# Optimization experiments

Measured on AMD Instinct MI355X. Metric: run time of the kernel, lower is better.

## Reference

```python
import jax, jax.numpy as jnp
import numpy as np

NUM_USERS = 100000
NUM_ITEMS = 50000
N_NODES = NUM_USERS + NUM_ITEMS
EMBED_DIM = 64
NUM_LAYERS = 3
N_EDGES = 1000000


def setup_inputs() -> dict:
    key = jax.random.key(0)
    k1, k2 = jax.random.split(key)
    edge_index = jax.random.randint(k1, (2, N_EDGES), 0, N_NODES, dtype=jnp.int64)
    # xavier_uniform for Embedding weight [N, d]
    limit = float(np.sqrt(6.0 / (N_NODES + EMBED_DIM)))
    emb_weight = jax.random.uniform(k2, (N_NODES, EMBED_DIM), dtype=jnp.float32,
                                    minval=-limit, maxval=limit)
    return {"edge_index": edge_index, "emb_weight": emb_weight}


def _lgconv(x, src, dst, norm):
    # out[dst] += norm * x[src]  (degree-normalized scatter-add)
    msgs = x[src] * norm[:, None]              # [E, d]
    return jax.ops.segment_sum(msgs, dst, num_segments=N_NODES)


def reference(edge_index, emb_weight):
    src, dst = edge_index[0], edge_index[1]
    # gcn_norm with add_self_loops=False: deg over target (col) index
    deg = jax.ops.segment_sum(jnp.ones((N_EDGES,), emb_weight.dtype), dst,
                              num_segments=N_NODES)
    dinv = jnp.where(deg > 0, jax.lax.rsqrt(jnp.maximum(deg, 1.0)), 0.0)
    norm = dinv[src] * dinv[dst]               # [E]

    emb = emb_weight
    acc = emb                                   # running sum over layer outputs
    for _ in range(NUM_LAYERS):
        emb = _lgconv(emb, src, dst, norm)
        acc = acc + emb
    out = acc / (NUM_LAYERS + 1)                # mean over stacked layer embeddings
    user_emb = out[:NUM_USERS]
    item_emb = out[NUM_USERS:]
    return (user_emb, item_emb)
```

## Files before the change

kernel.cpp:

```cpp
#include <hip/hip_runtime.h>
#include <hip/hip_fp16.h>


constexpr int kNodes     = 150000;
constexpr int kDim       = 64;
constexpr int kEdges     = 1000000;
constexpr int kEmbFloats = kNodes * kDim;
constexpr int kBkt       = (kNodes + 255) / 256;
constexpr int kBktCap    = 2048;
constexpr int kChunk     = 4096;

typedef float  floatx4 __attribute__((ext_vector_type(4)));

__device__ __forceinline__ int wave_incl_scan(int v, int lane) {
    #pragma unroll
    for (int s = 1; s < 64; s <<= 1) {
        int u = __shfl_up(v, s);
        if (lane >= s) v += u;
    }
    return v;
}

#define ACC_LO(s, r) asm("v_fma_mix_f32 %0, %1, 1.0, %0 op_sel:[0,0,0] op_sel_hi:[1,0,0]" : "+v"(s) : "v"(r))
#define ACC_HI(s, r) asm("v_fma_mix_f32 %0, %1, 1.0, %0 op_sel:[1,0,0] op_sel_hi:[1,0,0]" : "+v"(s) : "v"(r))

#define ACC_ROW(rr) do { \
    ACC_LO(s0, rr.x); ACC_HI(s1, rr.x); \
    ACC_LO(s2, rr.y); ACC_HI(s3, rr.y); \
    ACC_LO(s4, rr.z); ACC_HI(s5, rr.z); \
    ACC_LO(s6, rr.w); ACC_HI(s7, rr.w); } while (0)


__global__ __launch_bounds__(1024) void binA_kernel(const int* __restrict__ src,
                                                    const int* __restrict__ dst,
                                                    int* __restrict__ cur,
                                                    unsigned* __restrict__ bin) {
    __shared__ int hist[1024];
    __shared__ int cursor[1024];
    __shared__ int sexcl[1024];
    __shared__ int gstart[1024];
    __shared__ int wsum[16];
    __shared__ unsigned staged[kChunk];
    __shared__ unsigned short sbkt[kChunk];

    int t      = threadIdx.x;
    int lane   = t & 63;
    int w      = t >> 6;
    int chunk0 = blockIdx.x * kChunk;
    int n      = min(kChunk, kEdges - chunk0);

    hist[t] = 0;
    __syncthreads();

    int myb[4], myd[4];
    #pragma unroll
    for (int j = 0; j < 4; ++j) {
        int i = j * 1024 + t;
        if (i < n) {
            int d = dst[chunk0 + i];
            myb[j] = d >> 8;
            myd[j] = d & 255;
            atomicAdd(&hist[myb[j]], 1);
        } else myb[j] = -1;
    }
    __syncthreads();

    int c   = hist[t];
    int inc = wave_incl_scan(c, lane);
    if (lane == 63) wsum[w] = inc;
    __syncthreads();
    if (w == 0) {
        int v  = (lane < 16) ? wsum[lane] : 0;
        int sc = wave_incl_scan(v, lane);
        if (lane < 16) wsum[lane] = sc - v;
    }
    __syncthreads();
    int excl = wsum[w] + inc - c;
    sexcl[t]  = excl;
    cursor[t] = excl;
    if (t < kBkt) gstart[t] = atomicAdd(&cur[t], c);
    __syncthreads();

    #pragma unroll
    for (int j = 0; j < 4; ++j) {
        int i = j * 1024 + t;
        if (i < n) {
            int s = src[chunk0 + i];
            unsigned pk = ((unsigned)myd[j] << 24) | (unsigned)s;
            int p = atomicAdd(&cursor[myb[j]], 1);
            staged[p] = pk;
            sbkt[p]   = (unsigned short)myb[j];
        }
    }
    __syncthreads();

    #pragma unroll
    for (int j = 0; j < 4; ++j) {
        int i = j * 1024 + t;
        if (i < n) {
            int bu = sbkt[i];
            int gp = gstart[bu] + (i - sexcl[bu]);
            if (gp < kBktCap) bin[(size_t)bu * kBktCap + gp] = staged[i];
        }
    }
}


__global__ __launch_bounds__(256) void binB_kernel(const int* __restrict__ cur,
                                                   const unsigned* __restrict__ bin,
                                                   int* __restrict__ pairs,
                                                   int2* __restrict__ offcnt,
                                                   int* __restrict__ order,
                                                   const float4* __restrict__ emb4,
                                                   int4* __restrict__ y4) {
    __shared__ int lcnt[256];
    __shared__ int cursor[256];
    __shared__ int wsum[4];
    __shared__ int wred[4];
    __shared__ int chist[64];
    __shared__ int stage[kBktCap];
    __shared__ float sdinv[256];

    int b = blockIdx.x;
    int t = threadIdx.x;
    int lane = t & 63, w = t >> 6;
    int cnt = min(cur[b], kBktCap);
    const unsigned* mybin = bin + (size_t)b * kBktCap;

    {
        int acc = 0;
        for (int j = t; j < b; j += 256) acc += min(cur[j], kBktCap);
        #pragma unroll
        for (int s = 32; s; s >>= 1) acc += __shfl_down(acc, s);
        if (lane == 0) wred[w] = acc;
    }

    lcnt[t] = 0;
    if (t < 64) chist[t] = 0;
    __syncthreads();
    int bs = wred[0] + wred[1] + wred[2] + wred[3];

    for (int i = t; i < cnt; i += 256) atomicAdd(&lcnt[mybin[i] >> 24], 1);
    __syncthreads();

    int c   = lcnt[t];
    int inc = wave_incl_scan(c, lane);
    if (lane == 63) wsum[w] = inc;
    int cv = min(c, 63);
    atomicAdd(&chist[cv], 1);
    __syncthreads();

    if (t < 64) {
        int v  = chist[t];
        int sc = wave_incl_scan(v, lane);
        chist[t] = sc - v;
    }
    if (t == 0) {
        int a = 0;
        #pragma unroll
        for (int k = 0; k < 4; ++k) { int v = wsum[k]; wsum[k] = a; a += v; }
    }
    __syncthreads();
    int excl = wsum[w] + inc - c;

    int node = (b << 8) + t;
    float dv = (c > 0) ? rsqrtf((float)c) : 0.0f;
    sdinv[t] = dv;
    if (node < kNodes) offcnt[node] = make_int2(bs + excl, c);
    cursor[t] = excl;

    {
        int slot = atomicAdd(&chist[cv], 1);
        order[(b << 8) + slot] = (node < kNodes) ? node : kNodes;
    }
    __syncthreads();

    for (int i = t; i < cnt; i += 256) {
        unsigned v = mybin[i];
        int p = atomicAdd(&cursor[v >> 24], 1);
        stage[p] = (int)(v & 0x00FFFFFFu);
    }
    __syncthreads();
    for (int i = t; i < cnt; i += 256) pairs[bs + i] = stage[i];

    #pragma unroll
    for (int k = 0; k < 8; ++k) {
        int idx   = (k << 8) + t;
        int nl    = idx >> 3;
        int node2 = (b << 8) + nl;
        int qq    = idx & 7;
        if (node2 < kNodes) {
            float d = sdinv[nl];
            size_t e = (size_t)node2 * 16 + (size_t)qq * 2;
            float4 v0 = emb4[e];
            float4 v1 = emb4[e + 1];
            __half2 p0 = __floats2half2_rn(v0.x * d, v0.y * d);
            __half2 p1 = __floats2half2_rn(v0.z * d, v0.w * d);
            __half2 p2 = __floats2half2_rn(v1.x * d, v1.y * d);
            __half2 p3 = __floats2half2_rn(v1.z * d, v1.w * d);
            int4 wv;
            wv.x = *reinterpret_cast<int*>(&p0); wv.y = *reinterpret_cast<int*>(&p1);
            wv.z = *reinterpret_cast<int*>(&p2); wv.w = *reinterpret_cast<int*>(&p3);
            y4[(size_t)node2 * 8 + qq] = wv;
        } else if (node2 == kNodes) {
            int4 z; z.x = 0; z.y = 0; z.z = 0; z.w = 0;
            y4[(size_t)node2 * 8 + qq] = z;
        }
    }
}


__global__ __launch_bounds__(256) void gather_kernel(const int2* __restrict__ offcnt,
                                                     const int* __restrict__ order,
                                                     const int* __restrict__ pairs,
                                                     const __half* __restrict__ x16,
                                                     __half* __restrict__ yOut,
                                                     const float4* __restrict__ emb4,
                                                     const __half* __restrict__ y1,
                                                     const __half* __restrict__ y2,
                                                     float* __restrict__ outf,
                                                     int mode) {
    int t    = blockIdx.x * 256 + threadIdx.x;
    int slot = t >> 3;
    int q    = t & 7;
    int node = order[slot];
    if (node == kNodes) {
        if (mode == 0) {
            int4 z; z.x = 0; z.y = 0; z.z = 0; z.w = 0;
            ((int4*)(yOut + ((size_t)kNodes << 6)))[q] = z;
        }
        return;
    }
    int lane = threadIdx.x & 63;
    int gb   = lane & 56;

    int2 oc = offcnt[node];
    int b = oc.x, cnt = oc.y;

    float s0 = 0.f, s1 = 0.f, s2 = 0.f, s3 = 0.f,
          s4 = 0.f, s5 = 0.f, s6 = 0.f, s7 = 0.f;

    int mysrc = (q < cnt) ? pairs[b + q] : kNodes;
    for (int base2 = 0; base2 < cnt; base2 += 8) {
        int np  = base2 + 8 + q;
        int nxt = (np < cnt) ? pairs[b + np] : kNodes;

        int si0 = __shfl(mysrc, gb + 0);
        int si1 = __shfl(mysrc, gb + 1);
        int si2 = __shfl(mysrc, gb + 2);
        int si3 = __shfl(mysrc, gb + 3);
        int si4 = __shfl(mysrc, gb + 4);
        int si5 = __shfl(mysrc, gb + 5);
        int si6 = __shfl(mysrc, gb + 6);
        int si7 = __shfl(mysrc, gb + 7);
        int4 r0 = *(const int4*)(x16 + ((size_t)si0 << 6) + (q << 3));
        int4 r1 = *(const int4*)(x16 + ((size_t)si1 << 6) + (q << 3));
        int4 r2 = *(const int4*)(x16 + ((size_t)si2 << 6) + (q << 3));
        int4 r3 = *(const int4*)(x16 + ((size_t)si3 << 6) + (q << 3));
        int4 r4 = *(const int4*)(x16 + ((size_t)si4 << 6) + (q << 3));
        int4 r5 = *(const int4*)(x16 + ((size_t)si5 << 6) + (q << 3));
        int4 r6 = *(const int4*)(x16 + ((size_t)si6 << 6) + (q << 3));
        int4 r7 = *(const int4*)(x16 + ((size_t)si7 << 6) + (q << 3));
        ACC_ROW(r0); ACC_ROW(r1); ACC_ROW(r2); ACC_ROW(r3);
        ACC_ROW(r4); ACC_ROW(r5); ACC_ROW(r6); ACC_ROW(r7);
        mysrc = nxt;
    }

    float dv = (cnt > 0) ? rsqrtf((float)cnt) : 0.0f;
    if (mode == 0) {
        float dv2 = dv * dv;
        __half2 p0 = __floats2half2_rn(s0 * dv2, s1 * dv2);
        __half2 p1 = __floats2half2_rn(s2 * dv2, s3 * dv2);
        __half2 p2 = __floats2half2_rn(s4 * dv2, s5 * dv2);
        __half2 p3 = __floats2half2_rn(s6 * dv2, s7 * dv2);
        int4 wv;
        wv.x = *reinterpret_cast<int*>(&p0); wv.y = *reinterpret_cast<int*>(&p1);
        wv.z = *reinterpret_cast<int*>(&p2); wv.w = *reinterpret_cast<int*>(&p3);
        ((int4*)(yOut + ((size_t)node << 6)))[q] = wv;
    } else {
        float sq = sqrtf((float)cnt);
        size_t i4 = (size_t)node * 16 + (size_t)q * 2;
        int4 r1 = ((const int4*)(y1 + ((size_t)node << 6)))[q];
        int4 r2 = ((const int4*)(y2 + ((size_t)node << 6)))[q];
        float4 e0 = emb4[i4];
        float4 e1 = emb4[i4 + 1];
        float2 a0 = __half22float2(*reinterpret_cast<__half2*>(&r1.x));
        float2 a1 = __half22float2(*reinterpret_cast<__half2*>(&r1.y));
        float2 a2 = __half22float2(*reinterpret_cast<__half2*>(&r1.z));
        float2 a3 = __half22float2(*reinterpret_cast<__half2*>(&r1.w));
        float2 c0 = __half22float2(*reinterpret_cast<__half2*>(&r2.x));
        float2 c1 = __half22float2(*reinterpret_cast<__half2*>(&r2.y));
        float2 c2 = __half22float2(*reinterpret_cast<__half2*>(&r2.z));
        float2 c3 = __half22float2(*reinterpret_cast<__half2*>(&r2.w));
        floatx4 o0, o1;
        o0.x = (e0.x + (a0.x + c0.x) * sq + s0 * dv) * 0.25f;
        o0.y = (e0.y + (a0.y + c0.y) * sq + s1 * dv) * 0.25f;
        o0.z = (e0.z + (a1.x + c1.x) * sq + s2 * dv) * 0.25f;
        o0.w = (e0.w + (a1.y + c1.y) * sq + s3 * dv) * 0.25f;
        o1.x = (e1.x + (a2.x + c2.x) * sq + s4 * dv) * 0.25f;
        o1.y = (e1.y + (a2.y + c2.y) * sq + s5 * dv) * 0.25f;
        o1.z = (e1.z + (a3.x + c3.x) * sq + s6 * dv) * 0.25f;
        o1.w = (e1.w + (a3.y + c3.y) * sq + s7 * dv) * 0.25f;
        floatx4* op = (floatx4*)(outf + i4 * 4);
        __builtin_nontemporal_store(o0, op);
        __builtin_nontemporal_store(o1, op + 1);
    }
}


extern "C" void kernel_launch(void* const* d_in, const int* in_sizes, int n_in,
                              void* d_out, int out_size, void* d_ws, size_t ws_size,
                              hipStream_t stream) {
    const int*   edge  = (const int*)d_in[0];
    const int*   src   = edge;
    const int*   dst   = edge + kEdges;
    const float* emb_w = (const float*)d_in[1];
    float*       out   = (float*)d_out;

    char*     ws      = (char*)d_ws;
    int*      cur     = (int*)(ws);
    int*      order   = (int*)(ws + 4096);
    int2*     offcnt  = (int2*)(ws + 604160);
    int*      pairs   = (int*)(ws + 1804160);
    unsigned* bin     = (unsigned*)(ws + 5804160);
    __half*   y0      = (__half*)(ws + 10604672);
    __half*   yA      = (__half*)(ws + 29804800);
    __half*   yB      = (__half*)(ws + 49004928);

    const int binABlocks   = (kEdges + kChunk - 1) / kChunk;
    const int gatherBlocks = (kBkt * 256 * 8) / 256;

    (void)hipMemsetAsync(cur, 0, (size_t)kBkt * 4, stream);
    binA_kernel<<<binABlocks, 1024, 0, stream>>>(src, dst, cur, bin);
    binB_kernel<<<kBkt, 256, 0, stream>>>(cur, bin, pairs, offcnt, order,
                                          (const float4*)emb_w, (int4*)y0);

    gather_kernel<<<gatherBlocks, 256, 0, stream>>>(offcnt, order, pairs, y0,
                                                    yA, nullptr, nullptr, nullptr,
                                                    nullptr, 0);
    gather_kernel<<<gatherBlocks, 256, 0, stream>>>(offcnt, order, pairs, yA,
                                                    yB, nullptr, nullptr, nullptr,
                                                    nullptr, 0);
    gather_kernel<<<gatherBlocks, 256, 0, stream>>>(offcnt, order, pairs, yB,
                                                    nullptr, (const float4*)emb_w,
                                                    yA, yB, out, 1);
}
```

Measured before the change: 218.4 us.

## Fuse binB and gather layers into cooperative kernel with slot-ordered embeddings

Merges the bin-finalize pass and the three gather layers into one cooperative persistent kernel separated by grid-wide syncs, removing four launches. Embeddings are now stored in degree-sorted slot order and the edge source indices are remapped to slots, so gather reads and writes run sequentially per slot instead of indirecting through node ids. The cost is an extra remap pass over the edges, grid-sync overhead, and a persistent grid limited by occupancy. The workspace is also reshuffled so the bin buffer aliases yA.

Measured after the change: 714.6 us. 227% more time.

```diff
diff --git a/kernel.cpp b/kernel.cpp
--- a/kernel.cpp
+++ b/kernel.cpp
@@ -1,12 +1,15 @@
 #include <hip/hip_runtime.h>
 #include <hip/hip_fp16.h>
+#include <hip/hip_cooperative_groups.h>
+
+namespace cg = cooperative_groups;
 
 
 constexpr int kNodes     = 150000;
 constexpr int kDim       = 64;
 constexpr int kEdges     = 1000000;
-constexpr int kEmbFloats = kNodes * kDim;
 constexpr int kBkt       = (kNodes + 255) / 256;
+constexpr int kSlots     = kBkt * 256;
 constexpr int kBktCap    = 2048;
 constexpr int kChunk     = 4096;
 
@@ -106,13 +109,16 @@
 }
 
 
-__global__ __launch_bounds__(256) void binB_kernel(const int* __restrict__ cur,
-                                                   const unsigned* __restrict__ bin,
-                                                   int* __restrict__ pairs,
-                                                   int2* __restrict__ offcnt,
-                                                   int* __restrict__ order,
-                                                   const float4* __restrict__ emb4,
-                                                   int4* __restrict__ y4) {
+__device__ __forceinline__ void phaseB(int b,
+                                       const int* __restrict__ cur,
+                                       const unsigned* __restrict__ bin,
+                                       int* __restrict__ pairs,
+                                       int2* __restrict__ offcnt,
+                                       int* __restrict__ order,
+                                       int* __restrict__ islot,
+                                       int* __restrict__ totalE,
+                                       const float4* __restrict__ emb4,
+                                       int4* __restrict__ y4) {
     __shared__ int lcnt[256];
     __shared__ int cursor[256];
     __shared__ int wsum[4];
@@ -120,8 +126,8 @@
     __shared__ int chist[64];
     __shared__ int stage[kBktCap];
     __shared__ float sdinv[256];
-
-    int b = blockIdx.x;
+    __shared__ int sslot[256];
+
     int t = threadIdx.x;
     int lane = t & 63, w = t >> 6;
     int cnt = min(cur[b], kBktCap);
@@ -166,13 +172,15 @@
     int node = (b << 8) + t;
     float dv = (c > 0) ? rsqrtf((float)c) : 0.0f;
     sdinv[t] = dv;
-    if (node < kNodes) offcnt[node] = make_int2(bs + excl, c);
     cursor[t] = excl;
 
-    {
-        int slot = atomicAdd(&chist[cv], 1);
-        order[(b << 8) + slot] = (node < kNodes) ? node : kNodes;
-    }
+    int myslot = atomicAdd(&chist[cv], 1);
+    sslot[t] = myslot;
+    int gslot = (b << 8) + myslot;
+    order[gslot]  = (node < kNodes) ? node : kNodes;
+    offcnt[gslot] = make_int2(bs + excl, c);
+    if (node <= kNodes) islot[node] = gslot;
+    if (b == kBkt - 1 && t == 0) *totalE = bs + cnt;
     __syncthreads();
 
     for (int i = t; i < cnt; i += 256) {
@@ -187,8 +195,9 @@
     for (int k = 0; k < 8; ++k) {
         int idx   = (k << 8) + t;
         int nl    = idx >> 3;
+        int qq    = idx & 7;
         int node2 = (b << 8) + nl;
-        int qq    = idx & 7;
+        size_t gs = (size_t)((b << 8) + sslot[nl]);
         if (node2 < kNodes) {
             float d = sdinv[nl];
             size_t e = (size_t)node2 * 16 + (size_t)qq * 2;
@@ -201,110 +210,144 @@
             int4 wv;
             wv.x = *reinterpret_cast<int*>(&p0); wv.y = *reinterpret_cast<int*>(&p1);
             wv.z = *reinterpret_cast<int*>(&p2); wv.w = *reinterpret_cast<int*>(&p3);
-            y4[(size_t)node2 * 8 + qq] = wv;
-        } else if (node2 == kNodes) {
+            y4[gs * 8 + qq] = wv;
+        } else {
             int4 z; z.x = 0; z.y = 0; z.z = 0; z.w = 0;
-            y4[(size_t)node2 * 8 + qq] = z;
-        }
-    }
-}
-
-
-__global__ __launch_bounds__(256) void gather_kernel(const int2* __restrict__ offcnt,
-                                                     const int* __restrict__ order,
-                                                     const int* __restrict__ pairs,
-                                                     const __half* __restrict__ x16,
-                                                     __half* __restrict__ yOut,
-                                                     const float4* __restrict__ emb4,
-                                                     const __half* __restrict__ y1,
-                                                     const __half* __restrict__ y2,
-                                                     float* __restrict__ outf,
-                                                     int mode) {
-    int t    = blockIdx.x * 256 + threadIdx.x;
-    int slot = t >> 3;
-    int q    = t & 7;
-    int node = order[slot];
-    if (node == kNodes) {
-        if (mode == 0) {
-            int4 z; z.x = 0; z.y = 0; z.z = 0; z.w = 0;
-            ((int4*)(yOut + ((size_t)kNodes << 6)))[q] = z;
-        }
-        return;
-    }
+            y4[gs * 8 + qq] = z;
+        }
+    }
+}
+
+
+__device__ __forceinline__ void gather_layer(const int2* __restrict__ offcnt,
+                                             const int* __restrict__ order,
+                                             const int* __restrict__ pairs,
+                                             const __half* __restrict__ x16,
+                                             __half* __restrict__ yOut,
+                                             const float4* __restrict__ emb4,
+                                             const __half* __restrict__ y1,
+                                             const __half* __restrict__ y2,
+                                             float* __restrict__ outf,
+                                             int padslot, int mode) {
+    int q    = threadIdx.x & 7;
     int lane = threadIdx.x & 63;
     int gb   = lane & 56;
 
-    int2 oc = offcnt[node];
-    int b = oc.x, cnt = oc.y;
-
-    float s0 = 0.f, s1 = 0.f, s2 = 0.f, s3 = 0.f,
-          s4 = 0.f, s5 = 0.f, s6 = 0.f, s7 = 0.f;
-
-    int mysrc = (q < cnt) ? pairs[b + q] : kNodes;
-    for (int base2 = 0; base2 < cnt; base2 += 8) {
-        int np  = base2 + 8 + q;
-        int nxt = (np < cnt) ? pairs[b + np] : kNodes;
-
-        int si0 = __shfl(mysrc, gb + 0);
-        int si1 = __shfl(mysrc, gb + 1);
-        int si2 = __shfl(mysrc, gb + 2);
-        int si3 = __shfl(mysrc, gb + 3);
-        int si4 = __shfl(mysrc, gb + 4);
-        int si5 = __shfl(mysrc, gb + 5);
-        int si6 = __shfl(mysrc, gb + 6);
-        int si7 = __shfl(mysrc, gb + 7);
-        int4 r0 = *(const int4*)(x16 + ((size_t)si0 << 6) + (q << 3));
-        int4 r1 = *(const int4*)(x16 + ((size_t)si1 << 6) + (q << 3));
-        int4 r2 = *(const int4*)(x16 + ((size_t)si2 << 6) + (q << 3));
-        int4 r3 = *(const int4*)(x16 + ((size_t)si3 << 6) + (q << 3));
-        int4 r4 = *(const int4*)(x16 + ((size_t)si4 << 6) + (q << 3));
-        int4 r5 = *(const int4*)(x16 + ((size_t)si5 << 6) + (q << 3));
-        int4 r6 = *(const int4*)(x16 + ((size_t)si6 << 6) + (q << 3));
-        int4 r7 = *(const int4*)(x16 + ((size_t)si7 << 6) + (q << 3));
-        ACC_ROW(r0); ACC_ROW(r1); ACC_ROW(r2); ACC_ROW(r3);
-        ACC_ROW(r4); ACC_ROW(r5); ACC_ROW(r6); ACC_ROW(r7);
-        mysrc = nxt;
-    }
-
-    float dv = (cnt > 0) ? rsqrtf((float)cnt) : 0.0f;
-    if (mode == 0) {
-        float dv2 = dv * dv;
-        __half2 p0 = __floats2half2_rn(s0 * dv2, s1 * dv2);
-        __half2 p1 = __floats2half2_rn(s2 * dv2, s3 * dv2);
-        __half2 p2 = __floats2half2_rn(s4 * dv2, s5 * dv2);
-        __half2 p3 = __floats2half2_rn(s6 * dv2, s7 * dv2);
-        int4 wv;
-        wv.x = *reinterpret_cast<int*>(&p0); wv.y = *reinterpret_cast<int*>(&p1);
-        wv.z = *reinterpret_cast<int*>(&p2); wv.w = *reinterpret_cast<int*>(&p3);
-        ((int4*)(yOut + ((size_t)node << 6)))[q] = wv;
-    } else {
-        float sq = sqrtf((float)cnt);
-        size_t i4 = (size_t)node * 16 + (size_t)q * 2;
-        int4 r1 = ((const int4*)(y1 + ((size_t)node << 6)))[q];
-        int4 r2 = ((const int4*)(y2 + ((size_t)node << 6)))[q];
-        float4 e0 = emb4[i4];
-        float4 e1 = emb4[i4 + 1];
-        float2 a0 = __half22float2(*reinterpret_cast<__half2*>(&r1.x));
-        float2 a1 = __half22float2(*reinterpret_cast<__half2*>(&r1.y));
-        float2 a2 = __half22float2(*reinterpret_cast<__half2*>(&r1.z));
-        float2 a3 = __half22float2(*reinterpret_cast<__half2*>(&r1.w));
-        float2 c0 = __half22float2(*reinterpret_cast<__half2*>(&r2.x));
-        float2 c1 = __half22float2(*reinterpret_cast<__half2*>(&r2.y));
-        float2 c2 = __half22float2(*reinterpret_cast<__half2*>(&r2.z));
-        float2 c3 = __half22float2(*reinterpret_cast<__half2*>(&r2.w));
-        floatx4 o0, o1;
-        o0.x = (e0.x + (a0.x + c0.x) * sq + s0 * dv) * 0.25f;
-        o0.y = (e0.y + (a0.y + c0.y) * sq + s1 * dv) * 0.25f;
-        o0.z = (e0.z + (a1.x + c1.x) * sq + s2 * dv) * 0.25f;
-        o0.w = (e0.w + (a1.y + c1.y) * sq + s3 * dv) * 0.25f;
-        o1.x = (e1.x + (a2.x + c2.x) * sq + s4 * dv) * 0.25f;
-        o1.y = (e1.y + (a2.y + c2.y) * sq + s5 * dv) * 0.25f;
-        o1.z = (e1.z + (a3.x + c3.x) * sq + s6 * dv) * 0.25f;
-        o1.w = (e1.w + (a3.y + c3.y) * sq + s7 * dv) * 0.25f;
-        floatx4* op = (floatx4*)(outf + i4 * 4);
-        __builtin_nontemporal_store(o0, op);
-        __builtin_nontemporal_store(o1, op + 1);
-    }
+    for (int blk = blockIdx.x; blk < (kSlots >> 5); blk += gridDim.x) {
+        int slot = (blk << 5) + (threadIdx.x >> 3);
+
+        int2 oc = offcnt[slot];
+        int b = oc.x, cnt = oc.y;
+
+        float s0 = 0.f, s1 = 0.f, s2 = 0.f, s3 = 0.f,
+              s4 = 0.f, s5 = 0.f, s6 = 0.f, s7 = 0.f;
+
+        int mysrc = (q < cnt) ? pairs[b + q] : padslot;
+        for (int base2 = 0; base2 < cnt; base2 += 8) {
+            int np  = base2 + 8 + q;
+            int nxt = (np < cnt) ? pairs[b + np] : padslot;
+
+            int si0 = __shfl(mysrc, gb + 0);
+            int si1 = __shfl(mysrc, gb + 1);
+            int si2 = __shfl(mysrc, gb + 2);
+            int si3 = __shfl(mysrc, gb + 3);
+            int si4 = __shfl(mysrc, gb + 4);
+            int si5 = __shfl(mysrc, gb + 5);
+            int si6 = __shfl(mysrc, gb + 6);
+            int si7 = __shfl(mysrc, gb + 7);
+            int4 r0 = *(const int4*)(x16 + ((size_t)si0 << 6) + (q << 3));
+            int4 r1 = *(const int4*)(x16 + ((size_t)si1 << 6) + (q << 3));
+            int4 r2 = *(const int4*)(x16 + ((size_t)si2 << 6) + (q << 3));
+            int4 r3 = *(const int4*)(x16 + ((size_t)si3 << 6) + (q << 3));
+            int4 r4 = *(const int4*)(x16 + ((size_t)si4 << 6) + (q << 3));
+            int4 r5 = *(const int4*)(x16 + ((size_t)si5 << 6) + (q << 3));
+            int4 r6 = *(const int4*)(x16 + ((size_t)si6 << 6) + (q << 3));
+            int4 r7 = *(const int4*)(x16 + ((size_t)si7 << 6) + (q << 3));
+            ACC_ROW(r0); ACC_ROW(r1); ACC_ROW(r2); ACC_ROW(r3);
+            ACC_ROW(r4); ACC_ROW(r5); ACC_ROW(r6); ACC_ROW(r7);
+            mysrc = nxt;
+        }
+
+        if (mode == 0) {
+            float dvv = (cnt > 0) ? rsqrtf((float)cnt) : 0.0f;
+            float dv2 = dvv * dvv;
+            __half2 p0 = __floats2half2_rn(s0 * dv2, s1 * dv2);
+            __half2 p1 = __floats2half2_rn(s2 * dv2, s3 * dv2);
+            __half2 p2 = __floats2half2_rn(s4 * dv2, s5 * dv2);
+            __half2 p3 = __floats2half2_rn(s6 * dv2, s7 * dv2);
+            int4 wv;
+            wv.x = *reinterpret_cast<int*>(&p0); wv.y = *reinterpret_cast<int*>(&p1);
+            wv.z = *reinterpret_cast<int*>(&p2); wv.w = *reinterpret_cast<int*>(&p3);
+            ((int4*)(yOut + ((size_t)slot << 6)))[q] = wv;
+        } else {
+            int node = order[slot];
+            if (node < kNodes) {
+                float dvv = (cnt > 0) ? rsqrtf((float)cnt) : 0.0f;
+                float sq  = sqrtf((float)cnt);
+                int4 r1 = ((const int4*)(y1 + ((size_t)slot << 6)))[q];
+                int4 r2 = ((const int4*)(y2 + ((size_t)slot << 6)))[q];
+                size_t i4 = (size_t)node * 16 + (size_t)q * 2;
+                float4 e0 = emb4[i4];
+                float4 e1 = emb4[i4 + 1];
+                float2 a0 = __half22float2(*reinterpret_cast<__half2*>(&r1.x));
+                float2 a1 = __half22float2(*reinterpret_cast<__half2*>(&r1.y));
+                float2 a2 = __half22float2(*reinterpret_cast<__half2*>(&r1.z));
+                float2 a3 = __half22float2(*reinterpret_cast<__half2*>(&r1.w));
+                float2 c0 = __half22float2(*reinterpret_cast<__half2*>(&r2.x));
+                float2 c1 = __half22float2(*reinterpret_cast<__half2*>(&r2.y));
+                float2 c2 = __half22float2(*reinterpret_cast<__half2*>(&r2.z));
+                float2 c3 = __half22float2(*reinterpret_cast<__half2*>(&r2.w));
+                floatx4 o0, o1;
+                o0.x = (e0.x + (a0.x + c0.x) * sq + s0 * dvv) * 0.25f;
+                o0.y = (e0.y + (a0.y + c0.y) * sq + s1 * dvv) * 0.25f;
+                o0.z = (e0.z + (a1.x + c1.x) * sq + s2 * dvv) * 0.25f;
+                o0.w = (e0.w + (a1.y + c1.y) * sq + s3 * dvv) * 0.25f;
+                o1.x = (e1.x + (a2.x + c2.x) * sq + s4 * dvv) * 0.25f;
+                o1.y = (e1.y + (a2.y + c2.y) * sq + s5 * dvv) * 0.25f;
+                o1.z = (e1.z + (a3.x + c3.x) * sq + s6 * dvv) * 0.25f;
+                o1.w = (e1.w + (a3.y + c3.y) * sq + s7 * dvv) * 0.25f;
+                floatx4* op = (floatx4*)(outf + i4 * 4);
+                __builtin_nontemporal_store(o0, op);
+                __builtin_nontemporal_store(o1, op + 1);
+            }
+        }
+    }
+}
+
+
+__global__ __launch_bounds__(256, 8) void mega_kernel(const int* __restrict__ cur,
+                                                      const unsigned* __restrict__ bin,
+                                                      int* __restrict__ pairs,
+                                                      int2* __restrict__ offcnt,
+                                                      int* __restrict__ order,
+                                                      int* __restrict__ islot,
+                                                      int* __restrict__ totalE,
+                                                      const float4* __restrict__ emb4,
+                                                      int4* __restrict__ y0,
+                                                      __half* __restrict__ yA,
+                                                      __half* __restrict__ yB,
+                                                      float* __restrict__ outf) {
+    cg::grid_group grid = cg::this_grid();
+
+    for (int b = blockIdx.x; b < kBkt; b += gridDim.x)
+        phaseB(b, cur, bin, pairs, offcnt, order, islot, totalE, emb4, y0);
+    grid.sync();
+
+    int E = *totalE;
+    int padslot = islot[kNodes];
+    for (int i = blockIdx.x * 256 + threadIdx.x; i < E; i += gridDim.x * 256)
+        pairs[i] = islot[pairs[i]];
+    grid.sync();
+
+    const __half* y0h = (const __half*)y0;
+    gather_layer(offcnt, order, pairs, y0h, yA, nullptr, nullptr, nullptr, nullptr,
+                 padslot, 0);
+    grid.sync();
+    gather_layer(offcnt, order, pairs, yA, yB, nullptr, nullptr, nullptr, nullptr,
+                 padslot, 0);
+    grid.sync();
+    gather_layer(offcnt, order, pairs, yB, nullptr, emb4, yA, yB, outf,
+                 padslot, 1);
 }
 
 
@@ -317,31 +360,37 @@
     const float* emb_w = (const float*)d_in[1];
     float*       out   = (float*)d_out;
 
-    char*     ws      = (char*)d_ws;
-    int*      cur     = (int*)(ws);
-    int*      order   = (int*)(ws + 4096);
-    int2*     offcnt  = (int2*)(ws + 604160);
-    int*      pairs   = (int*)(ws + 1804160);
-    unsigned* bin     = (unsigned*)(ws + 5804160);
-    __half*   y0      = (__half*)(ws + 10604672);
-    __half*   yA      = (__half*)(ws + 29804800);
-    __half*   yB      = (__half*)(ws + 49004928);
-
-    const int binABlocks   = (kEdges + kChunk - 1) / kChunk;
-    const int gatherBlocks = (kBkt * 256 * 8) / 256;
+    char*     ws     = (char*)d_ws;
+    int*      cur    = (int*)(ws);
+    int*      totalE = (int*)(ws + 4096);
+    int*      islot  = (int*)(ws + 4224);
+    int*      order  = (int*)(ws + 604288);
+    int2*     offcnt = (int2*)(ws + 1204352);
+    int*      pairs  = (int*)(ws + 2404480);
+    int4*     y0     = (int4*)(ws + 6404480);
+    __half*   yB     = (__half*)(ws + 25606528);
+    unsigned* bin    = (unsigned*)(ws + 44808576);
+    __half*   yA     = (__half*)(ws + 44808576);
+
+    const int binABlocks = (kEdges + kChunk - 1) / kChunk;
+
+    static int coopGrid = 0;
+    if (coopGrid == 0) {
+        int nb = 0;
+        (void)hipOccupancyMaxActiveBlocksPerMultiprocessor(&nb, mega_kernel, 256, 0);
+        if (nb < 1) nb = 1;
+        long g = (long)nb * 256;
+        if (g > (kSlots >> 5)) g = (kSlots >> 5);
+        coopGrid = (int)g;
+    }
 
     (void)hipMemsetAsync(cur, 0, (size_t)kBkt * 4, stream);
     binA_kernel<<<binABlocks, 1024, 0, stream>>>(src, dst, cur, bin);
-    binB_kernel<<<kBkt, 256, 0, stream>>>(cur, bin, pairs, offcnt, order,
-                                          (const float4*)emb_w, (int4*)y0);
-
-    gather_kernel<<<gatherBlocks, 256, 0, stream>>>(offcnt, order, pairs, y0,
-                                                    yA, nullptr, nullptr, nullptr,
-                                                    nullptr, 0);
-    gather_kernel<<<gatherBlocks, 256, 0, stream>>>(offcnt, order, pairs, yA,
-                                                    yB, nullptr, nullptr, nullptr,
-                                                    nullptr, 0);
-    gather_kernel<<<gatherBlocks, 256, 0, stream>>>(offcnt, order, pairs, yB,
-                                                    nullptr, (const float4*)emb_w,
-                                                    yA, yB, out, 1);
-}
+
+    const float4* emb4 = (const float4*)emb_w;
+    void* margs[] = { (void*)&cur, (void*)&bin, (void*)&pairs, (void*)&offcnt,
+                      (void*)&order, (void*)&islot, (void*)&totalE, (void*)&emb4,
+                      (void*)&y0, (void*)&yA, (void*)&yB, (void*)&out };
+    (void)hipLaunchCooperativeKernel(mega_kernel, dim3(coopGrid), dim3(256),
+                                     margs, 0, stream);
+}
```

## Replace two-pass bucket binning with global-atomic counting-sort CSR build

Applied to the files above, without the earlier changes.

Replaces the binA/binB bucketed sort (LDS-staged per-chunk binning into fixed-capacity buckets) with a global degree histogram, a block-partial prefix sum, a per-node offset build, and a scatter kernel that places each source via a global atomic cursor. This drops the intermediate bin buffer and its kBktCap truncation. In exchange it uses 2M global atomics on a 150k-entry array, adds kernel launches, and makes the edge order within each row nondeterministic, which can change the fp16 accumulation order.

Result: slower. 324.6 us (+48.6%).

```diff
diff --git a/kernel.cpp b/kernel.cpp
--- a/kernel.cpp
+++ b/kernel.cpp
@@ -2,15 +2,13 @@
 #include <hip/hip_fp16.h>
 
 
-constexpr int kNodes     = 150000;
-constexpr int kDim       = 64;
-constexpr int kEdges     = 1000000;
-constexpr int kEmbFloats = kNodes * kDim;
-constexpr int kBkt       = (kNodes + 255) / 256;
-constexpr int kBktCap    = 2048;
-constexpr int kChunk     = 4096;
-
-typedef float  floatx4 __attribute__((ext_vector_type(4)));
+constexpr int kNodes = 150000;
+constexpr int kDim   = 64;
+constexpr int kEdges = 1000000;
+constexpr int kBkt   = (kNodes + 255) / 256;
+constexpr int kSlots = kBkt * 256;
+
+typedef float floatx4 __attribute__((ext_vector_type(4)));
 
 __device__ __forceinline__ int wave_incl_scan(int v, int lane) {
     #pragma unroll
@@ -31,119 +29,66 @@
     ACC_LO(s6, rr.w); ACC_HI(s7, rr.w); } while (0)
 
 
-__global__ __launch_bounds__(1024) void binA_kernel(const int* __restrict__ src,
-                                                    const int* __restrict__ dst,
-                                                    int* __restrict__ cur,
-                                                    unsigned* __restrict__ bin) {
-    __shared__ int hist[1024];
-    __shared__ int cursor[1024];
-    __shared__ int sexcl[1024];
-    __shared__ int gstart[1024];
-    __shared__ int wsum[16];
-    __shared__ unsigned staged[kChunk];
-    __shared__ unsigned short sbkt[kChunk];
-
-    int t      = threadIdx.x;
-    int lane   = t & 63;
-    int w      = t >> 6;
-    int chunk0 = blockIdx.x * kChunk;
-    int n      = min(kChunk, kEdges - chunk0);
-
-    hist[t] = 0;
-    __syncthreads();
-
-    int myb[4], myd[4];
-    #pragma unroll
-    for (int j = 0; j < 4; ++j) {
-        int i = j * 1024 + t;
-        if (i < n) {
-            int d = dst[chunk0 + i];
-            myb[j] = d >> 8;
-            myd[j] = d & 255;
-            atomicAdd(&hist[myb[j]], 1);
-        } else myb[j] = -1;
-    }
-    __syncthreads();
-
-    int c   = hist[t];
-    int inc = wave_incl_scan(c, lane);
-    if (lane == 63) wsum[w] = inc;
-    __syncthreads();
-    if (w == 0) {
-        int v  = (lane < 16) ? wsum[lane] : 0;
-        int sc = wave_incl_scan(v, lane);
-        if (lane < 16) wsum[lane] = sc - v;
-    }
-    __syncthreads();
-    int excl = wsum[w] + inc - c;
-    sexcl[t]  = excl;
-    cursor[t] = excl;
-    if (t < kBkt) gstart[t] = atomicAdd(&cur[t], c);
-    __syncthreads();
-
-    #pragma unroll
-    for (int j = 0; j < 4; ++j) {
-        int i = j * 1024 + t;
-        if (i < n) {
-            int s = src[chunk0 + i];
-            unsigned pk = ((unsigned)myd[j] << 24) | (unsigned)s;
-            int p = atomicAdd(&cursor[myb[j]], 1);
-            staged[p] = pk;
-            sbkt[p]   = (unsigned short)myb[j];
-        }
-    }
-    __syncthreads();
-
-    #pragma unroll
-    for (int j = 0; j < 4; ++j) {
-        int i = j * 1024 + t;
-        if (i < n) {
-            int bu = sbkt[i];
-            int gp = gstart[bu] + (i - sexcl[bu]);
-            if (gp < kBktCap) bin[(size_t)bu * kBktCap + gp] = staged[i];
-        }
-    }
-}
-
-
-__global__ __launch_bounds__(256) void binB_kernel(const int* __restrict__ cur,
-                                                   const unsigned* __restrict__ bin,
-                                                   int* __restrict__ pairs,
-                                                   int2* __restrict__ offcnt,
-                                                   int* __restrict__ order,
-                                                   const float4* __restrict__ emb4,
-                                                   int4* __restrict__ y4) {
-    __shared__ int lcnt[256];
-    __shared__ int cursor[256];
+__global__ __launch_bounds__(256) void hist_kernel(const int* __restrict__ dst,
+                                                   int* __restrict__ deg) {
+    int i = blockIdx.x * 1024 + threadIdx.x;
+    #pragma unroll
+    for (int j = 0; j < 4; ++j, i += 256)
+        if (i < kEdges) atomicAdd(&deg[dst[i]], 1);
+}
+
+
+__global__ __launch_bounds__(256) void psum_kernel(const int* __restrict__ deg,
+                                                   int* __restrict__ psum) {
+    __shared__ int wr[4];
+    int base = blockIdx.x * 1024;
+    int acc = 0;
+    for (int j = threadIdx.x; j < 1024; j += 256) {
+        int n = base + j;
+        acc += (n < kNodes) ? deg[n] : 0;
+    }
+    int lane = threadIdx.x & 63, w = threadIdx.x >> 6;
+    #pragma unroll
+    for (int s = 32; s; s >>= 1) acc += __shfl_down(acc, s);
+    if (lane == 0) wr[w] = acc;
+    __syncthreads();
+    if (threadIdx.x == 0) psum[blockIdx.x] = wr[0] + wr[1] + wr[2] + wr[3];
+}
+
+
+__global__ __launch_bounds__(256) void buildB_kernel(const int* __restrict__ deg,
+                                                     const int* __restrict__ psum,
+                                                     int2* __restrict__ offcnt,
+                                                     int* __restrict__ order,
+                                                     int* __restrict__ gcursor,
+                                                     const float4* __restrict__ emb4,
+                                                     int4* __restrict__ y4) {
     __shared__ int wsum[4];
     __shared__ int wred[4];
     __shared__ int chist[64];
-    __shared__ int stage[kBktCap];
     __shared__ float sdinv[256];
 
     int b = blockIdx.x;
     int t = threadIdx.x;
     int lane = t & 63, w = t >> 6;
-    int cnt = min(cur[b], kBktCap);
-    const unsigned* mybin = bin + (size_t)b * kBktCap;
+    int nstart = b << 8;
+    int node = nstart + t;
+    int c = (node < kNodes) ? deg[node] : 0;
 
     {
+        int pchunks = nstart >> 10;
+        int rem0 = pchunks << 10;
         int acc = 0;
-        for (int j = t; j < b; j += 256) acc += min(cur[j], kBktCap);
+        for (int j = t; j < pchunks; j += 256) acc += psum[j];
+        for (int j = rem0 + t; j < nstart; j += 256) acc += deg[j];
         #pragma unroll
         for (int s = 32; s; s >>= 1) acc += __shfl_down(acc, s);
         if (lane == 0) wred[w] = acc;
     }
-
-    lcnt[t] = 0;
     if (t < 64) chist[t] = 0;
     __syncthreads();
     int bs = wred[0] + wred[1] + wred[2] + wred[3];
 
-    for (int i = t; i < cnt; i += 256) atomicAdd(&lcnt[mybin[i] >> 24], 1);
-    __syncthreads();
-
-    int c   = lcnt[t];
     int inc = wave_incl_scan(c, lane);
     if (lane == 63) wsum[w] = inc;
     int cv = min(c, 63);
@@ -163,32 +108,23 @@
     __syncthreads();
     int excl = wsum[w] + inc - c;
 
-    int node = (b << 8) + t;
     float dv = (c > 0) ? rsqrtf((float)c) : 0.0f;
     sdinv[t] = dv;
-    if (node < kNodes) offcnt[node] = make_int2(bs + excl, c);
-    cursor[t] = excl;
-
-    {
-        int slot = atomicAdd(&chist[cv], 1);
-        order[(b << 8) + slot] = (node < kNodes) ? node : kNodes;
-    }
-    __syncthreads();
-
-    for (int i = t; i < cnt; i += 256) {
-        unsigned v = mybin[i];
-        int p = atomicAdd(&cursor[v >> 24], 1);
-        stage[p] = (int)(v & 0x00FFFFFFu);
-    }
-    __syncthreads();
-    for (int i = t; i < cnt; i += 256) pairs[bs + i] = stage[i];
+    if (node < kNodes) {
+        offcnt[node]  = make_int2(bs + excl, c);
+        gcursor[node] = bs + excl;
+    }
+
+    int myslot = atomicAdd(&chist[cv], 1);
+    order[nstart + myslot] = (node < kNodes) ? node : kNodes;
+    __syncthreads();
 
     #pragma unroll
     for (int k = 0; k < 8; ++k) {
         int idx   = (k << 8) + t;
         int nl    = idx >> 3;
-        int node2 = (b << 8) + nl;
         int qq    = idx & 7;
+        int node2 = nstart + nl;
         if (node2 < kNodes) {
             float d = sdinv[nl];
             size_t e = (size_t)node2 * 16 + (size_t)qq * 2;
@@ -203,10 +139,23 @@
             wv.z = *reinterpret_cast<int*>(&p2); wv.w = *reinterpret_cast<int*>(&p3);
             y4[(size_t)node2 * 8 + qq] = wv;
         } else if (node2 == kNodes) {
-            int4 z; z.x = 0; z.y = 0; z.z = 0; z.w = 0;
-            y4[(size_t)node2 * 8 + qq] = z;
+            y4[(size_t)node2 * 8 + qq] = make_int4(0, 0, 0, 0);
         }
     }
+}
+
+
+__global__ __launch_bounds__(256) void scatter_kernel(const int* __restrict__ src,
+                                                      const int* __restrict__ dst,
+                                                      int* __restrict__ gcursor,
+                                                      int* __restrict__ pairs) {
+    int i = blockIdx.x * 1024 + threadIdx.x;
+    #pragma unroll
+    for (int j = 0; j < 4; ++j, i += 256)
+        if (i < kEdges) {
+            int p = atomicAdd(&gcursor[dst[i]], 1);
+            pairs[p] = src[i];
+        }
 }
 
 
@@ -226,7 +175,7 @@
     int node = order[slot];
     if (node == kNodes) {
         if (mode == 0) {
-            int4 z; z.x = 0; z.y = 0; z.z = 0; z.w = 0;
+            int4 z = make_int4(0, 0, 0, 0);
             ((int4*)(yOut + ((size_t)kNodes << 6)))[q] = z;
         }
         return;
@@ -317,31 +266,35 @@
     const float* emb_w = (const float*)d_in[1];
     float*       out   = (float*)d_out;
 
-    char*     ws      = (char*)d_ws;
-    int*      cur     = (int*)(ws);
-    int*      order   = (int*)(ws + 4096);
-    int2*     offcnt  = (int2*)(ws + 604160);
-    int*      pairs   = (int*)(ws + 1804160);
-    unsigned* bin     = (unsigned*)(ws + 5804160);
-    __half*   y0      = (__half*)(ws + 10604672);
-    __half*   yA      = (__half*)(ws + 29804800);
-    __half*   yB      = (__half*)(ws + 49004928);
-
-    const int binABlocks   = (kEdges + kChunk - 1) / kChunk;
-    const int gatherBlocks = (kBkt * 256 * 8) / 256;
-
-    (void)hipMemsetAsync(cur, 0, (size_t)kBkt * 4, stream);
-    binA_kernel<<<binABlocks, 1024, 0, stream>>>(src, dst, cur, bin);
-    binB_kernel<<<kBkt, 256, 0, stream>>>(cur, bin, pairs, offcnt, order,
-                                          (const float4*)emb_w, (int4*)y0);
-
-    gather_kernel<<<gatherBlocks, 256, 0, stream>>>(offcnt, order, pairs, y0,
-                                                    yA, nullptr, nullptr, nullptr,
-                                                    nullptr, 0);
-    gather_kernel<<<gatherBlocks, 256, 0, stream>>>(offcnt, order, pairs, yA,
-                                                    yB, nullptr, nullptr, nullptr,
-                                                    nullptr, 0);
-    gather_kernel<<<gatherBlocks, 256, 0, stream>>>(offcnt, order, pairs, yB,
-                                                    nullptr, (const float4*)emb_w,
-                                                    yA, yB, out, 1);
-}
+    char*   ws      = (char*)d_ws;
+    int*    deg     = (int*)(ws);
+    int*    psum    = (int*)(ws + 600064);
+    int*    gcursor = (int*)(ws + 601088);
+    int*    order   = (int*)(ws + 1201152);
+    int2*   offcnt  = (int2*)(ws + 1801216);
+    int*    pairs   = (int*)(ws + 3001344);
+    __half* y0      = (__half*)(ws + 7001344);
+    __half* yA      = (__half*)(ws + 26201472);
+    __half* yB      = (__half*)(ws + 45401600);
+
+    const int edgeBlks   = (kEdges + 1023) / 1024;
+    const int psumBlks   = (kNodes + 1023) / 1024;
+    const int gatherBlks = (kSlots * 8) / 256;
+
+    (void)hipMemsetAsync(deg, 0, (size_t)kNodes * 4, stream);
+    hist_kernel<<<edgeBlks, 256, 0, stream>>>(dst, deg);
+    psum_kernel<<<psumBlks, 256, 0, stream>>>(deg, psum);
+    buildB_kernel<<<kBkt, 256, 0, stream>>>(deg, psum, offcnt, order, gcursor,
+                                            (const float4*)emb_w, (int4*)y0);
+    scatter_kernel<<<edgeBlks, 256, 0, stream>>>(src, dst, gcursor, pairs);
+
+    gather_kernel<<<gatherBlks, 256, 0, stream>>>(offcnt, order, pairs, y0,
+                                                  yA, nullptr, nullptr, nullptr,
+                                                  nullptr, 0);
+    gather_kernel<<<gatherBlks, 256, 0, stream>>>(offcnt, order, pairs, yA,
+                                                  yB, nullptr, nullptr, nullptr,
+                                                  nullptr, 0);
+    gather_kernel<<<gatherBlks, 256, 0, stream>>>(offcnt, order, pairs, yB,
+                                                  nullptr, (const float4*)emb_w,
+                                                  yA, yB, out, 1);
+}
```
